# Performance work log

Measured on AMD Instinct MI355X. Metric: run time of the kernel, lower is better.

## Reference

```python
import jax, jax.numpy as jnp
import numpy as np
import math

EMBED_DIM = 1024
NUM_HEADS = 16
HEAD_DIM = EMBED_DIM // NUM_HEADS


def setup_inputs() -> dict:
    key = jax.random.key(0)
    ks = jax.random.split(key, 9)
    B, S, D = 4, 2048, EMBED_DIM
    s = 1.0 / math.sqrt(D)
    x = jax.random.normal(ks[0], (B, S, D), dtype=jnp.float32)
    Wq = jax.random.normal(ks[1], (D, D), dtype=jnp.float32) * s
    bq = jnp.zeros((D,), dtype=jnp.float32)
    Wk = jax.random.normal(ks[2], (D, D), dtype=jnp.float32) * s
    bk = jnp.zeros((D,), dtype=jnp.float32)
    Wv = jax.random.normal(ks[3], (D, D), dtype=jnp.float32) * s
    bv = jnp.zeros((D,), dtype=jnp.float32)
    Wo = jax.random.normal(ks[4], (D, D), dtype=jnp.float32) * s
    bo = jnp.zeros((D,), dtype=jnp.float32)
    return {"x": x, "Wq": Wq, "bq": bq, "Wk": Wk, "bk": bk,
            "Wv": Wv, "bv": bv, "Wo": Wo, "bo": bo}


def reference(x, Wq, bq, Wk, bk, Wv, bv, Wo, bo):
    B, S, D = x.shape
    H, hd = NUM_HEADS, HEAD_DIM
    # projections: [B,S,D] -> [B,H,S,hd]
    def split_heads(t):
        return t.reshape(B, S, H, hd).transpose(0, 2, 1, 3)
    Q = split_heads(x @ Wq + bq)
    K = split_heads(x @ Wk + bk)
    V = split_heads(x @ Wv + bv)
    scale = 1.0 / math.sqrt(hd)
    scores = jnp.einsum('bhqd,bhkd->bhqk', Q, K) * scale  # [B,H,S,S]
    causal = jnp.tril(jnp.ones((S, S), dtype=bool))
    scores = jnp.where(causal, scores, -jnp.inf)
    attn = jax.nn.softmax(scores, axis=-1)
    out = jnp.einsum('bhqk,bhkd->bhqd', attn, V)  # [B,H,S,hd]
    out = out.transpose(0, 2, 1, 3).reshape(B, S, D)
    return out @ Wo + bo
```

## Files before the change

### kernel.cpp

```cpp
#include <hip/hip_runtime.h>
#include <hip/hip_bf16.h>
#include <cstdint>
#include <cstddef>

typedef __bf16 bf16_t;
typedef __bf16 bf16x4 __attribute__((ext_vector_type(4)));
typedef __bf16 bf16x8 __attribute__((ext_vector_type(8)));
typedef float f32x4 __attribute__((ext_vector_type(4)));
typedef float f32x16 __attribute__((ext_vector_type(16)));
typedef unsigned u32x2 __attribute__((ext_vector_type(2)));

typedef __attribute__((address_space(1))) void as1_void_t;
typedef __attribute__((address_space(3))) void as3_void_t;

__device__ __forceinline__ void gload_lds16(const bf16_t* g, bf16_t* l) {
  __builtin_amdgcn_global_load_lds((as1_void_t*)g, (as3_void_t*)l, 16, 0, 0);
}

__global__ __launch_bounds__(256) void prep_k(
    const float* __restrict__ x,
    const float* __restrict__ wq, const float* __restrict__ wk,
    const float* __restrict__ wv, const float* __restrict__ wo,
    bf16_t* __restrict__ xb, bf16_t* __restrict__ wqt,
    bf16_t* __restrict__ wkt, bf16_t* __restrict__ wvt, bf16_t* __restrict__ wot)
{
  __shared__ float t[64][65];
  if (blockIdx.x < 2048) {
    const int tid = blockIdx.x * 256 + threadIdx.x;
    const int NX4 = (8192 * 1024) / 4;
    for (int i = tid; i < NX4; i += 2048 * 256) {
      float4 v = ((const float4*)x)[i];
      bf16x4 o;
      o[0] = (bf16_t)v.x; o[1] = (bf16_t)v.y; o[2] = (bf16_t)v.z; o[3] = (bf16_t)v.w;
      ((bf16x4*)xb)[i] = o;
    }
  } else {
    const int tile = blockIdx.x - 2048;
    const int tr = tile >> 4, tc = tile & 15;
    const int c = threadIdx.x & 63, r4 = threadIdx.x >> 6;
#pragma unroll 1
    for (int zz = 0; zz < 4; ++zz) {
      const float* w = (zz == 0) ? wq : (zz == 1) ? wk : (zz == 2) ? wv : wo;
      bf16_t* wt = (zz == 0) ? wqt : (zz == 1) ? wkt : (zz == 2) ? wvt : wot;
#pragma unroll
      for (int rr = 0; rr < 16; ++rr) {
        int row = rr * 4 + r4;
        t[row][c] = w[(size_t)(tr * 64 + row) * 1024 + tc * 64 + c];
      }
      __syncthreads();
#pragma unroll
      for (int rr = 0; rr < 16; ++rr) {
        int row = rr * 4 + r4;
        wt[(size_t)(tc * 64 + row) * 1024 + tr * 64 + c] = (bf16_t)t[c][row];
      }
      __syncthreads();
    }
  }
}

constexpr int BM = 128, BN = 128, BK = 64;

template <int MODE>
__global__ __launch_bounds__(256) void gemm_proj_k(
    const bf16_t* __restrict__ A,
    const bf16_t* __restrict__ W0T, const bf16_t* __restrict__ W1T,
    const float* __restrict__ b0, const float* __restrict__ b1,
    bf16_t* __restrict__ o0, bf16_t* __restrict__ o1)
{
  constexpr int K = 1024;
  __shared__ bf16_t a_lds[BM * BK];
  __shared__ bf16_t b_lds[BN * BK];
  const int z = blockIdx.z;
  const bf16_t* Bt = (z == 0) ? W0T : W1T;
  const float* bias = (z == 0) ? b0 : b1;
  bf16_t* outp = (z == 0) ? o0 : o1;
  const float oscale = (MODE == 0 && z == 0) ? 0.18033688011112042f : 1.0f;

  const int tid = threadIdx.x;
  const int l = tid & 63;
  const int wv = tid >> 6;
  const int wr = wv >> 1, wc = wv & 1;
  const int lr = l & 15, lg = l >> 4;
  const int bm = blockIdx.x * BM;
  const int bn = blockIdx.y * BN;

  f32x4 acc[4][4] = {};

  const int srow = tid >> 3;
  const int scc = tid & 7;

  for (int k0 = 0; k0 < K; k0 += BK) {
    __syncthreads();
#pragma unroll
    for (int it = 0; it < 4; ++it) {
      int row = srow + it * 32;
      int gk = (scc ^ (row & 7)) * 8;
      gload_lds16(A + (size_t)(bm + row) * K + k0 + gk, a_lds + row * BK + scc * 8);
      gload_lds16(Bt + (size_t)(bn + row) * K + k0 + gk, b_lds + row * BK + scc * 8);
    }
    __syncthreads();
#pragma unroll
    for (int kk = 0; kk < 2; ++kk) {
      bf16x8 af[4], bfr[4];
#pragma unroll
      for (int m = 0; m < 4; ++m) {
        int row = wr * 64 + m * 16 + lr;
        int ch = (kk * 4 + lg) ^ (row & 7);
        af[m] = *(const bf16x8*)&a_lds[row * BK + ch * 8];
      }
#pragma unroll
      for (int n = 0; n < 4; ++n) {
        int row = wc * 64 + n * 16 + lr;
        int ch = (kk * 4 + lg) ^ (row & 7);
        bfr[n] = *(const bf16x8*)&b_lds[row * BK + ch * 8];
      }
#pragma unroll
      for (int m = 0; m < 4; ++m)
#pragma unroll
        for (int n = 0; n < 4; ++n) {
          if constexpr (MODE == 0)
            acc[m][n] = __builtin_amdgcn_mfma_f32_16x16x32_bf16(bfr[n], af[m], acc[m][n], 0, 0, 0);
          else
            acc[m][n] = __builtin_amdgcn_mfma_f32_16x16x32_bf16(af[m], bfr[n], acc[m][n], 0, 0, 0);
        }
    }
  }

  if constexpr (MODE == 0) {
#pragma unroll
    for (int m = 0; m < 4; ++m) {
      const int row = bm + wr * 64 + m * 16 + lr;
      const int bhb = row >> 11, seq = row & 2047;
#pragma unroll
      for (int n = 0; n < 4; ++n) {
        const int col0 = bn + wc * 64 + n * 16 + lg * 4;
        const float4 b4 = *(const float4*)&bias[col0];
        const int bh = bhb * 16 + (col0 >> 6);
        const int dl0 = col0 & 63;
        size_t off = (((size_t)(bh * 64 + (seq >> 5)) * 4 + (dl0 >> 4)) * 64
                      + (((dl0 >> 3) & 1) * 32 + (seq & 31))) * 8 + (dl0 & 7);
        bf16x4 o4;
        o4[0] = (bf16_t)((acc[m][n][0] + b4.x) * oscale);
        o4[1] = (bf16_t)((acc[m][n][1] + b4.y) * oscale);
        o4[2] = (bf16_t)((acc[m][n][2] + b4.z) * oscale);
        o4[3] = (bf16_t)((acc[m][n][3] + b4.w) * oscale);
        *(bf16x4*)&outp[off] = o4;
      }
    }
  } else {
#pragma unroll
    for (int n = 0; n < 4; ++n) {
      const int col = bn + wc * 64 + n * 16 + lr;
      const float bv_ = bias[col];
      const int dl = col & 63;
#pragma unroll
      for (int m = 0; m < 4; ++m) {
        const int row0 = bm + wr * 64 + m * 16 + lg * 4;
        const int bhb = row0 >> 11, seq0 = row0 & 2047;
        const int bh = bhb * 16 + (col >> 6);
        size_t off = ((((size_t)(bh * 64 + (seq0 >> 5)) * 2 + (dl >> 5)) * 2
                       + ((seq0 >> 4) & 1)) * 64
                      + (((seq0 >> 3) & 1) * 32 + (dl & 31))) * 8 + (seq0 & 7);
        bf16x4 o4;
        o4[0] = (bf16_t)(acc[m][n][0] + bv_);
        o4[1] = (bf16_t)(acc[m][n][1] + bv_);
        o4[2] = (bf16_t)(acc[m][n][2] + bv_);
        o4[3] = (bf16_t)(acc[m][n][3] + bv_);
        *(bf16x4*)&outp[off] = o4;
      }
    }
  }
}

__global__ __launch_bounds__(256) void gemm_o_k(
    const bf16_t* __restrict__ A, const bf16_t* __restrict__ Bt,
    const float* __restrict__ bias, float* __restrict__ outp)
{
  constexpr int K = 1024;
  __shared__ bf16_t a_lds[BM * BK];
  __shared__ bf16_t b_lds[BN * BK];
  const int tid = threadIdx.x;
  const int l = tid & 63;
  const int wv = tid >> 6;
  const int wr = wv >> 1, wc = wv & 1;
  const int lr = l & 15, lg = l >> 4;
  const int bm = blockIdx.x * BM;
  const int bn = blockIdx.y * BN;

  f32x4 acc[4][4] = {};
  const int srow = tid >> 3;
  const int scc = tid & 7;

  for (int k0 = 0; k0 < K; k0 += BK) {
    __syncthreads();
#pragma unroll
    for (int it = 0; it < 4; ++it) {
      int row = srow + it * 32;
      int gk = (scc ^ (row & 7)) * 8;
      gload_lds16(A + (size_t)(bm + row) * K + k0 + gk, a_lds + row * BK + scc * 8);
      gload_lds16(Bt + (size_t)(bn + row) * K + k0 + gk, b_lds + row * BK + scc * 8);
    }
    __syncthreads();
#pragma unroll
    for (int kk = 0; kk < 2; ++kk) {
      bf16x8 af[4], bfr[4];
#pragma unroll
      for (int m = 0; m < 4; ++m) {
        int row = wr * 64 + m * 16 + lr;
        int ch = (kk * 4 + lg) ^ (row & 7);
        af[m] = *(const bf16x8*)&a_lds[row * BK + ch * 8];
      }
#pragma unroll
      for (int n = 0; n < 4; ++n) {
        int row = wc * 64 + n * 16 + lr;
        int ch = (kk * 4 + lg) ^ (row & 7);
        bfr[n] = *(const bf16x8*)&b_lds[row * BK + ch * 8];
      }
#pragma unroll
      for (int m = 0; m < 4; ++m)
#pragma unroll
        for (int n = 0; n < 4; ++n)
          acc[m][n] = __builtin_amdgcn_mfma_f32_16x16x32_bf16(bfr[n], af[m], acc[m][n], 0, 0, 0);
    }
  }

#pragma unroll
  for (int m = 0; m < 4; ++m) {
    const int row = bm + wr * 64 + m * 16 + lr;
#pragma unroll
    for (int n = 0; n < 4; ++n) {
      const int col0 = bn + wc * 64 + n * 16 + lg * 4;
      const float4 b4 = *(const float4*)&bias[col0];
      float4 o4;
      o4.x = acc[m][n][0] + b4.x;
      o4.y = acc[m][n][1] + b4.y;
      o4.z = acc[m][n][2] + b4.z;
      o4.w = acc[m][n][3] + b4.w;
      *(float4*)&outp[(size_t)row * 1024 + col0] = o4;
    }
  }
}

__device__ __forceinline__ unsigned pack2bf(float a, float b) {
  union { bf16_t h[2]; unsigned u; } z;
  z.h[0] = (bf16_t)a; z.h[1] = (bf16_t)b;
  return z.u;
}

__device__ __forceinline__ void permswap(unsigned& a, unsigned& b) {
  u32x2 r = __builtin_amdgcn_permlane32_swap(a, b, false, false);
  a = r[0]; b = r[1];
}

__device__ __forceinline__ float xadd32(float x) {
  unsigned a = __float_as_uint(x), b = __float_as_uint(x);
  permswap(a, b);
  return __uint_as_float(a) + __uint_as_float(b);
}

__device__ __forceinline__ void sm_pv(
    const f32x16& st, const bf16x8 vf[2][2], f32x16 oacc[2], float& ls)
{
  float p[16];
#pragma unroll
  for (int r = 0; r < 16; ++r) p[r] = __builtin_amdgcn_exp2f(st[r]);
  float s0 = (p[0] + p[1]) + (p[2] + p[3]);
  float s1 = (p[4] + p[5]) + (p[6] + p[7]);
  float s2 = (p[8] + p[9]) + (p[10] + p[11]);
  float s3 = (p[12] + p[13]) + (p[14] + p[15]);
  ls += ((s0 + s1) + (s2 + s3));

  bf16x8 pf[2];
#pragma unroll
  for (int ks = 0; ks < 2; ++ks) {
    unsigned a0 = pack2bf(p[8 * ks + 0], p[8 * ks + 1]);
    unsigned a1 = pack2bf(p[8 * ks + 2], p[8 * ks + 3]);
    unsigned b0 = pack2bf(p[8 * ks + 4], p[8 * ks + 5]);
    unsigned b1 = pack2bf(p[8 * ks + 6], p[8 * ks + 7]);
    permswap(a0, b0);
    permswap(a1, b1);
    union { unsigned wd[4]; bf16x8 v; } zz;
    zz.wd[0] = a0; zz.wd[1] = a1; zz.wd[2] = b0; zz.wd[3] = b1;
    pf[ks] = zz.v;
  }
  __builtin_amdgcn_s_setprio(1);
#pragma unroll
  for (int dt = 0; dt < 2; ++dt)
#pragma unroll
    for (int ks = 0; ks < 2; ++ks)
      oacc[dt] = __builtin_amdgcn_mfma_f32_32x32x16_bf16(vf[dt][ks], pf[ks], oacc[dt], 0, 0, 0);
  __builtin_amdgcn_s_setprio(0);
}

__global__ __launch_bounds__(256) void attn_k(
    const bf16_t* __restrict__ Q, const bf16_t* __restrict__ Kmat,
    const bf16_t* __restrict__ Vt, bf16_t* __restrict__ O)
{
  const int bh = blockIdx.x;
  const int by = 15 - blockIdx.y;
  const int tid = threadIdx.x;
  const int l = tid & 63;
  const int w = tid >> 6;
  const int t = 4 * by + w;
  const int NP = 2 * by + 2;
  const int qb = t * 32;
  const int lc = l & 31;
  const int hi = l >> 5;

  __shared__ bf16_t kbuf[2][4096];
  __shared__ bf16_t vbuf[2][4096];

  const bf16_t* Kg = Kmat + (size_t)bh * 131072;
  const bf16_t* Vg = Vt + (size_t)bh * 131072;
  const bf16_t* Qf = Q + (size_t)bh * 131072 + l * 8;

  bf16x8 qf[4];
#pragma unroll
  for (int ds = 0; ds < 4; ++ds)
    qf[ds] = *(const bf16x8*)&Qf[(size_t)(t * 4 + ds) * 512];

  float ls = 0.f;
  f32x16 oa[2] = {};

  auto stage = [&](int p, int slot) {
    const bf16_t* kg = Kg + (size_t)p * 4096 + tid * 8;
    const bf16_t* vg = Vg + (size_t)p * 4096 + tid * 8;
    gload_lds16(kg,        &kbuf[slot][tid * 8]);
    gload_lds16(kg + 2048, &kbuf[slot][2048 + tid * 8]);
    gload_lds16(vg,        &vbuf[slot][tid * 8]);
    gload_lds16(vg + 2048, &vbuf[slot][2048 + tid * 8]);
  };

  auto dotile = [&](const bf16_t* kb, const bf16_t* vb, int s) {
    bf16x8 kf[4];
#pragma unroll
    for (int ds = 0; ds < 4; ++ds) kf[ds] = *(const bf16x8*)&kb[ds * 512];
    bf16x8 vf[2][2];
#pragma unroll
    for (int dt = 0; dt < 2; ++dt)
#pragma unroll
      for (int ks = 0; ks < 2; ++ks)
        vf[dt][ks] = *(const bf16x8*)&vb[(dt * 2 + ks) * 512];

    f32x16 st = {};
    __builtin_amdgcn_s_setprio(1);
#pragma unroll
    for (int ds = 0; ds < 4; ++ds)
      st = __builtin_amdgcn_mfma_f32_32x32x16_bf16(kf[ds], qf[ds], st, 0, 0, 0);
    __builtin_amdgcn_s_setprio(0);
    if (s == t) {
#pragma unroll
      for (int r = 0; r < 16; ++r) {
        int kvloc = (r & 3) + 8 * (r >> 2) + 4 * hi;
        if (kvloc > lc) st[r] = -1e30f;
      }
    }
    sm_pv(st, vf, oa, ls);
  };

  stage(0, 0);

  for (int p = 0; p < NP; ++p) {
    asm volatile("s_waitcnt vmcnt(0)" ::: "memory");
    __builtin_amdgcn_s_barrier();
    __builtin_amdgcn_sched_barrier(0);
    if (p + 1 < NP) stage(p + 1, (p + 1) & 1);

    const int s0 = 2 * p;
    const bf16_t* kb = &kbuf[p & 1][l * 8];
    const bf16_t* vb = &vbuf[p & 1][l * 8];
    if (s0 <= t) dotile(kb, vb, s0);
    if (s0 + 1 <= t) dotile(kb + 2048, vb + 2048, s0 + 1);
  }

  const int b = bh >> 4, h = bh & 15;
  const float inv = 1.0f / xadd32(ls);
  const size_t rowoff = (size_t)(b * 2048 + qb + lc) * 1024 + h * 64;
#pragma unroll
  for (int dt = 0; dt < 2; ++dt)
#pragma unroll
    for (int g = 0; g < 4; ++g) {
      bf16x4 o4;
#pragma unroll
      for (int tt = 0; tt < 4; ++tt) o4[tt] = (bf16_t)(oa[dt][g * 4 + tt] * inv);
      *(bf16x4*)&O[rowoff + dt * 32 + g * 8 + hi * 4] = o4;
    }
}

extern "C" void kernel_launch(void* const* d_in, const int* in_sizes, int n_in,
                              void* d_out, int out_size, void* d_ws, size_t ws_size,
                              hipStream_t stream)
{
  (void)in_sizes; (void)n_in; (void)out_size; (void)ws_size;
  const float* x  = (const float*)d_in[0];
  const float* Wq = (const float*)d_in[1];
  const float* bq = (const float*)d_in[2];
  const float* Wk = (const float*)d_in[3];
  const float* bk = (const float*)d_in[4];
  const float* Wv = (const float*)d_in[5];
  const float* bv = (const float*)d_in[6];
  const float* Wo = (const float*)d_in[7];
  const float* bo = (const float*)d_in[8];

  char* ws = (char*)d_ws;
  bf16_t* xb   = (bf16_t*)(ws);
  bf16_t* wqt  = (bf16_t*)(ws + (size_t)(16u << 20));
  bf16_t* wkt  = (bf16_t*)(ws + (size_t)(18u << 20));
  bf16_t* wvt  = (bf16_t*)(ws + (size_t)(20u << 20));
  bf16_t* wot  = (bf16_t*)(ws + (size_t)(22u << 20));
  bf16_t* qws  = (bf16_t*)(ws + (size_t)(24u << 20));
  bf16_t* kws  = (bf16_t*)(ws + (size_t)(40u << 20));
  bf16_t* vtws = (bf16_t*)(ws + (size_t)(56u << 20));

  prep_k<<<2304, 256, 0, stream>>>(x, Wq, Wk, Wv, Wo, xb, wqt, wkt, wvt, wot);

  dim3 gqk(8192 / BM, 1024 / BN, 2);
  gemm_proj_k<0><<<gqk, 256, 0, stream>>>(xb, wqt, wkt, bq, bk, qws, kws);
  dim3 gv(8192 / BM, 1024 / BN, 1);
  gemm_proj_k<1><<<gv, 256, 0, stream>>>(xb, wvt, wvt, bv, bv, vtws, vtws);

  attn_k<<<dim3(64, 16), 256, 0, stream>>>(qws, kws, vtws, xb);

  dim3 go(8192 / BM, 1024 / BN);
  gemm_o_k<<<go, 256, 0, stream>>>(xb, wot, bo, (float*)d_out);
}
```

Before: 176.6 us.

## Double-buffer GEMM LDS tiles with BK=32 and merge GEMM kernels

The projection and output GEMMs now share one templated kernel that double-buffers LDS tiles. K steps shrink from 64 to 32, so the next tile's global-to-LDS load is issued while the current tile feeds the MFMAs, with a single waitcnt plus barrier per step. A new pair-row swizzle keeps LDS reads conflict-free at the narrower K step. The aim is to hide global load latency behind compute, at the cost of twice as many loop iterations and barriers.

After: 202.1 us. +14.4%, slower.

```diff
diff --git a/kernel.cpp b/kernel.cpp
--- a/kernel.cpp
+++ b/kernel.cpp
@@ -58,23 +58,23 @@
   }
 }
 
-constexpr int BM = 128, BN = 128, BK = 64;
-
-template <int MODE>
-__global__ __launch_bounds__(256) void gemm_proj_k(
+constexpr int BM = 128, BN = 128;
+
+template <int EPI>
+__global__ __launch_bounds__(256) void gemm_k(
     const bf16_t* __restrict__ A,
     const bf16_t* __restrict__ W0T, const bf16_t* __restrict__ W1T,
     const float* __restrict__ b0, const float* __restrict__ b1,
-    bf16_t* __restrict__ o0, bf16_t* __restrict__ o1)
-{
-  constexpr int K = 1024;
-  __shared__ bf16_t a_lds[BM * BK];
-  __shared__ bf16_t b_lds[BN * BK];
+    void* __restrict__ o0v, void* __restrict__ o1v)
+{
+  constexpr int K = 1024, NSTEP = 32;
+  __shared__ bf16_t a_lds[2][4096];
+  __shared__ bf16_t b_lds[2][4096];
   const int z = blockIdx.z;
-  const bf16_t* Bt = (z == 0) ? W0T : W1T;
-  const float* bias = (z == 0) ? b0 : b1;
-  bf16_t* outp = (z == 0) ? o0 : o1;
-  const float oscale = (MODE == 0 && z == 0) ? 0.18033688011112042f : 1.0f;
+  const bf16_t* Bt = z ? W1T : W0T;
+  const float* bias = z ? b1 : b0;
+  void* outv = z ? o1v : o0v;
+  const float oscale = (EPI == 0 && z == 0) ? 0.18033688011112042f : 1.0f;
 
   const int tid = threadIdx.x;
   const int l = tid & 63;
@@ -86,47 +86,62 @@
 
   f32x4 acc[4][4] = {};
 
-  const int srow = tid >> 3;
-  const int scc = tid & 7;
-
-  for (int k0 = 0; k0 < K; k0 += BK) {
-    __syncthreads();
-#pragma unroll
-    for (int it = 0; it < 4; ++it) {
-      int row = srow + it * 32;
-      int gk = (scc ^ (row & 7)) * 8;
-      gload_lds16(A + (size_t)(bm + row) * K + k0 + gk, a_lds + row * BK + scc * 8);
-      gload_lds16(Bt + (size_t)(bn + row) * K + k0 + gk, b_lds + row * BK + scc * 8);
-    }
-    __syncthreads();
-#pragma unroll
-    for (int kk = 0; kk < 2; ++kk) {
-      bf16x8 af[4], bfr[4];
-#pragma unroll
-      for (int m = 0; m < 4; ++m) {
-        int row = wr * 64 + m * 16 + lr;
-        int ch = (kk * 4 + lg) ^ (row & 7);
-        af[m] = *(const bf16x8*)&a_lds[row * BK + ch * 8];
-      }
+  const int sp = tid >> 3;
+  const int sc = tid & 7;
+
+  auto stage = [&](int ks, int slot) {
+    const int k0 = ks * 32;
+#pragma unroll
+    for (int r = 0; r < 2; ++r) {
+      int p = r * 32 + sp;
+      int gk = sc ^ (p & 7);
+      int grow = 2 * p + (gk >> 2);
+      int gcol = (gk & 3) * 8;
+      gload_lds16(A + (size_t)(bm + grow) * K + k0 + gcol,
+                  &a_lds[slot][r * 2048 + tid * 8]);
+      gload_lds16(Bt + (size_t)(bn + grow) * K + k0 + gcol,
+                  &b_lds[slot][r * 2048 + tid * 8]);
+    }
+  };
+
+  stage(0, 0);
+
+  for (int ks = 0; ks < NSTEP; ++ks) {
+    asm volatile("s_waitcnt vmcnt(0)" ::: "memory");
+    __builtin_amdgcn_s_barrier();
+    __builtin_amdgcn_sched_barrier(0);
+    if (ks + 1 < NSTEP) stage(ks + 1, (ks + 1) & 1);
+
+    const bf16_t* al = a_lds[ks & 1];
+    const bf16_t* bl = b_lds[ks & 1];
+    bf16x8 af[4], bfr[4];
+#pragma unroll
+    for (int m = 0; m < 4; ++m) {
+      int row = wr * 64 + m * 16 + lr;
+      int pair = row >> 1;
+      int ch = (((row & 1) << 2) + lg) ^ (pair & 7);
+      af[m] = *(const bf16x8*)&al[pair * 64 + ch * 8];
+    }
+#pragma unroll
+    for (int n = 0; n < 4; ++n) {
+      int row = wc * 64 + n * 16 + lr;
+      int pair = row >> 1;
+      int ch = (((row & 1) << 2) + lg) ^ (pair & 7);
+      bfr[n] = *(const bf16x8*)&bl[pair * 64 + ch * 8];
+    }
+#pragma unroll
+    for (int m = 0; m < 4; ++m)
 #pragma unroll
       for (int n = 0; n < 4; ++n) {
-        int row = wc * 64 + n * 16 + lr;
-        int ch = (kk * 4 + lg) ^ (row & 7);
-        bfr[n] = *(const bf16x8*)&b_lds[row * BK + ch * 8];
-      }
-#pragma unroll
-      for (int m = 0; m < 4; ++m)
-#pragma unroll
-        for (int n = 0; n < 4; ++n) {
-          if constexpr (MODE == 0)
-            acc[m][n] = __builtin_amdgcn_mfma_f32_16x16x32_bf16(bfr[n], af[m], acc[m][n], 0, 0, 0);
-          else
-            acc[m][n] = __builtin_amdgcn_mfma_f32_16x16x32_bf16(af[m], bfr[n], acc[m][n], 0, 0, 0);
-        }
-    }
-  }
-
-  if constexpr (MODE == 0) {
+        if constexpr (EPI == 1)
+          acc[m][n] = __builtin_amdgcn_mfma_f32_16x16x32_bf16(af[m], bfr[n], acc[m][n], 0, 0, 0);
+        else
+          acc[m][n] = __builtin_amdgcn_mfma_f32_16x16x32_bf16(bfr[n], af[m], acc[m][n], 0, 0, 0);
+      }
+  }
+
+  if constexpr (EPI == 0) {
+    bf16_t* outp = (bf16_t*)outv;
 #pragma unroll
     for (int m = 0; m < 4; ++m) {
       const int row = bm + wr * 64 + m * 16 + lr;
@@ -147,7 +162,8 @@
         *(bf16x4*)&outp[off] = o4;
       }
     }
-  } else {
+  } else if constexpr (EPI == 1) {
+    bf16_t* outp = (bf16_t*)outv;
 #pragma unroll
     for (int n = 0; n < 4; ++n) {
       const int col = bn + wc * 64 + n * 16 + lr;
@@ -169,74 +185,22 @@
         *(bf16x4*)&outp[off] = o4;
       }
     }
-  }
-}
-
-__global__ __launch_bounds__(256) void gemm_o_k(
-    const bf16_t* __restrict__ A, const bf16_t* __restrict__ Bt,
-    const float* __restrict__ bias, float* __restrict__ outp)
-{
-  constexpr int K = 1024;
-  __shared__ bf16_t a_lds[BM * BK];
-  __shared__ bf16_t b_lds[BN * BK];
-  const int tid = threadIdx.x;
-  const int l = tid & 63;
-  const int wv = tid >> 6;
-  const int wr = wv >> 1, wc = wv & 1;
-  const int lr = l & 15, lg = l >> 4;
-  const int bm = blockIdx.x * BM;
-  const int bn = blockIdx.y * BN;
-
-  f32x4 acc[4][4] = {};
-  const int srow = tid >> 3;
-  const int scc = tid & 7;
-
-  for (int k0 = 0; k0 < K; k0 += BK) {
-    __syncthreads();
-#pragma unroll
-    for (int it = 0; it < 4; ++it) {
-      int row = srow + it * 32;
-      int gk = (scc ^ (row & 7)) * 8;
-      gload_lds16(A + (size_t)(bm + row) * K + k0 + gk, a_lds + row * BK + scc * 8);
-      gload_lds16(Bt + (size_t)(bn + row) * K + k0 + gk, b_lds + row * BK + scc * 8);
-    }
-    __syncthreads();
-#pragma unroll
-    for (int kk = 0; kk < 2; ++kk) {
-      bf16x8 af[4], bfr[4];
-#pragma unroll
-      for (int m = 0; m < 4; ++m) {
-        int row = wr * 64 + m * 16 + lr;
-        int ch = (kk * 4 + lg) ^ (row & 7);
-        af[m] = *(const bf16x8*)&a_lds[row * BK + ch * 8];
-      }
+  } else {
+    float* outp = (float*)outv;
+#pragma unroll
+    for (int m = 0; m < 4; ++m) {
+      const int row = bm + wr * 64 + m * 16 + lr;
 #pragma unroll
       for (int n = 0; n < 4; ++n) {
-        int row = wc * 64 + n * 16 + lr;
-        int ch = (kk * 4 + lg) ^ (row & 7);
-        bfr[n] = *(const bf16x8*)&b_lds[row * BK + ch * 8];
-      }
-#pragma unroll
-      for (int m = 0; m < 4; ++m)
-#pragma unroll
-        for (int n = 0; n < 4; ++n)
-          acc[m][n] = __builtin_amdgcn_mfma_f32_16x16x32_bf16(bfr[n], af[m], acc[m][n], 0, 0, 0);
-    }
-  }
-
-#pragma unroll
-  for (int m = 0; m < 4; ++m) {
-    const int row = bm + wr * 64 + m * 16 + lr;
-#pragma unroll
-    for (int n = 0; n < 4; ++n) {
-      const int col0 = bn + wc * 64 + n * 16 + lg * 4;
-      const float4 b4 = *(const float4*)&bias[col0];
-      float4 o4;
-      o4.x = acc[m][n][0] + b4.x;
-      o4.y = acc[m][n][1] + b4.y;
-      o4.z = acc[m][n][2] + b4.z;
-      o4.w = acc[m][n][3] + b4.w;
-      *(float4*)&outp[(size_t)row * 1024 + col0] = o4;
+        const int col0 = bn + wc * 64 + n * 16 + lg * 4;
+        const float4 b4 = *(const float4*)&bias[col0];
+        float4 o4;
+        o4.x = acc[m][n][0] + b4.x;
+        o4.y = acc[m][n][1] + b4.y;
+        o4.z = acc[m][n][2] + b4.z;
+        o4.w = acc[m][n][3] + b4.w;
+        *(float4*)&outp[(size_t)row * 1024 + col0] = o4;
+      }
     }
   }
 }
@@ -415,12 +379,11 @@
   prep_k<<<2304, 256, 0, stream>>>(x, Wq, Wk, Wv, Wo, xb, wqt, wkt, wvt, wot);
 
   dim3 gqk(8192 / BM, 1024 / BN, 2);
-  gemm_proj_k<0><<<gqk, 256, 0, stream>>>(xb, wqt, wkt, bq, bk, qws, kws);
-  dim3 gv(8192 / BM, 1024 / BN, 1);
-  gemm_proj_k<1><<<gv, 256, 0, stream>>>(xb, wvt, wvt, bv, bv, vtws, vtws);
+  gemm_k<0><<<gqk, 256, 0, stream>>>(xb, wqt, wkt, bq, bk, qws, kws);
+  dim3 g1(8192 / BM, 1024 / BN, 1);
+  gemm_k<1><<<g1, 256, 0, stream>>>(xb, wvt, wvt, bv, bv, vtws, vtws);
 
   attn_k<<<dim3(64, 16), 256, 0, stream>>>(qws, kws, vtws, xb);
 
-  dim3 go(8192 / BM, 1024 / BN);
-  gemm_o_k<<<go, 256, 0, stream>>>(xb, wot, bo, (float*)d_out);
-}
+  gemm_k<2><<<g1, 256, 0, stream>>>(xb, wot, wot, bo, bo, d_out, d_out);
+}
```
